# Optimization experiments

Measured on AMD Instinct MI355X. Metric: run time of the kernel, lower is better.

## Reference

```python
import jax, jax.numpy as jnp
import numpy as np

N, E, B = 524288, 4194304, 16384
F_IN, FP, TV, GOUT = 14, 1024, 256, 32
EPS = 1e-5
SLOPE = 0.2  # PyG GATConv default negative_slope


def setup_inputs() -> dict:
    key = jax.random.key(0)
    ks = iter(jax.random.split(key, 64))
    def nrm(shape, scale=1.0):
        return jax.random.normal(next(ks), shape, dtype=jnp.float32) * scale
    def uni(shape, lo, hi):
        return jax.random.uniform(next(ks), shape, dtype=jnp.float32, minval=lo, maxval=hi)
    def bn(d):  # [gamma, beta, running_mean, running_var]
        return jnp.stack([uni((d,), 0.5, 1.5), nrm((d,), 0.1), nrm((d,), 0.1), uni((d,), 0.5, 1.5)])
    return {
        'x': nrm((N, F_IN)),
        'edge_index': jax.random.randint(next(ks), (2, E), 0, N, dtype=jnp.int32),
        'batch': jnp.sort(jax.random.randint(next(ks), (N,), 0, B, dtype=jnp.int32)),
        'fingerprint': nrm((B, FP)),
        'transformer_features': nrm((B, TV)),
        'W1': nrm((F_IN, F_IN), 0.3), 'a_src1': nrm((F_IN,), 0.3), 'a_dst1': nrm((F_IN,), 0.3), 'b1': nrm((F_IN,), 0.1),
        'W2': nrm((F_IN, GOUT), 0.3), 'a_src2': nrm((GOUT,), 0.3), 'a_dst2': nrm((GOUT,), 0.3), 'b2': nrm((GOUT,), 0.1),
        'fc1_w': nrm((FP, 400), 0.04), 'fc1_b': nrm((400,), 0.1), 'bn1': bn(400),
        'fc2_w': nrm((400, 200), 0.07), 'fc2_b': nrm((200,), 0.1), 'bn2': bn(200),
        'fc3_w': nrm((TV, 400), 0.08), 'fc3_b': nrm((400,), 0.1), 'bn3': bn(400),
        'fc4_w': nrm((400, 200), 0.07), 'fc4_b': nrm((200,), 0.1), 'bn4': bn(200),
        'fcc1_w': nrm((GOUT + 400, 100), 0.07), 'fcc1_b': nrm((100,), 0.1), 'bnc': bn(100),
        'fcc2_w': nrm((100, 1), 0.1), 'fcc2_b': nrm((1,), 0.1),
    }


def _bn(h, p):  # eval-mode BatchNorm1d with packed params [4, d]
    return (h - p[2]) * jax.lax.rsqrt(p[3] + EPS) * p[0] + p[1]


def _gat(x, W, a_s, a_d, b, src, dst, n):
    # PyG GATConv, heads=1: messages flow src -> dst, softmax over incoming edges per dst
    h = x @ W                                   # [n, C]
    e = jax.nn.leaky_relu((h @ a_s)[src] + (h @ a_d)[dst], SLOPE)  # [E_tot]
    m = jax.lax.stop_gradient(jax.ops.segment_max(e, dst, num_segments=n))
    w = jnp.exp(e - m[dst])
    denom = jax.ops.segment_sum(w, dst, num_segments=n)
    alpha = w / denom[dst]
    out = jax.ops.segment_sum(alpha[:, None] * h[src], dst, num_segments=n)
    return out + b


def reference(x, edge_index, batch, fingerprint, transformer_features,
              W1, a_src1, a_dst1, b1, W2, a_src2, a_dst2, b2,
              fc1_w, fc1_b, bn1, fc2_w, fc2_b, bn2,
              fc3_w, fc3_b, bn3, fc4_w, fc4_b, bn4,
              fcc1_w, fcc1_b, bnc, fcc2_w, fcc2_b):
    n = x.shape[0]
    loop = jnp.arange(n, dtype=edge_index.dtype)  # add_self_loops
    src = jnp.concatenate([edge_index[0], loop])
    dst = jnp.concatenate([edge_index[1], loop])
    g = jax.nn.relu(_gat(x, W1, a_src1, a_dst1, b1, src, dst, n))
    g = jax.nn.relu(_gat(g, W2, a_src2, a_dst2, b2, src, dst, n))
    pool = jax.ops.segment_sum(g, batch, num_segments=B)  # global_add_pool -> [B, GOUT]
    fp = jax.nn.relu(_bn(fingerprint @ fc1_w + fc1_b, bn1))
    fp = jax.nn.relu(_bn(fp @ fc2_w + fc2_b, bn2))
    tv = jax.nn.relu(_bn(transformer_features @ fc3_w + fc3_b, bn3))
    tv = jax.nn.relu(_bn(tv @ fc4_w + fc4_b, bn4))
    comb = jnp.concatenate([pool, fp, tv], axis=1)  # [B, 32+200+200]
    comb = jax.nn.relu(_bn(comb @ fcc1_w + fcc1_b, bnc))
    return comb @ fcc2_w + fcc2_b  # [B, 1]
```

## Files before the change

### kernel.cpp

```cpp
#include <hip/hip_runtime.h>

typedef unsigned short u16;
typedef unsigned int u32;
typedef __attribute__((ext_vector_type(8))) short bf16x8;
typedef __attribute__((ext_vector_type(4))) float f32x4;

#define N_NODES 524288
#define N_EDGES 4194304
#define N_GRAPH 16384
#define P_BLOCKS 1024
#define BKTS 512
#define DPB 1024
#define CAP 8960
#define TTOT 2825
#define LBLK 2048

__device__ __forceinline__ float bf2f(u16 u){ u32 x=((u32)u)<<16; float f; __builtin_memcpy(&f,&x,4); return f; }
__device__ __forceinline__ float lo2f(u32 u){ u32 x=u<<16; float f; __builtin_memcpy(&f,&x,4); return f; }
__device__ __forceinline__ float hi2f(u32 u){ u32 x=u&0xffff0000u; float f; __builtin_memcpy(&f,&x,4); return f; }
__device__ __forceinline__ u16 f2bf(float f){ u32 x; __builtin_memcpy(&x,&f,4); return (u16)((x + 0x7fffu + ((x>>16)&1u))>>16); }
__device__ __forceinline__ float lrelu(float e){ return e>0.f? e : 0.2f*e; }
__device__ __forceinline__ float gload(const void* p, int i, int is32){
    return is32 ? ((const float*)p)[i] : bf2f(((const u16*)p)[i]);
}
__device__ __forceinline__ u32 fmax_key(float f){ u32 u; __builtin_memcpy(&u,&f,4); return (u>>31)? ~u : (u|0x80000000u); }
__device__ __forceinline__ float key_fmax(u32 k){ u32 u = (k>>31)? (k^0x80000000u) : ~k; float f; __builtin_memcpy(&f,&u,4); return f; }

__device__ __forceinline__ void edge_acc(uint4 q0, uint4 q1, float adv, float M,
        float* acc, float& den){
    float as_; __builtin_memcpy(&as_, &q1.w, 4);
    float w = __expf(lrelu(as_ + adv) - M); den += w;
    u32 u[7] = {q0.x,q0.y,q0.z,q0.w,q1.x,q1.y,q1.z};
    #pragma unroll
    for (int f=0;f<14;f++){ u32 uu=u[f>>1]; acc[f] += w*((f&1)? hi2f(uu):lo2f(uu)); }
}

__device__ __forceinline__ void walk8(const int* __restrict__ ssrc, const u16* __restrict__ hsrc,
        int beg, int end, float adv, float M, float* acc, float& den){
    for (int j = beg; j < end; j += 8){
        int s8[8];
        #pragma unroll
        for (int k=0;k<8;k++){
            int e = j + k;
            s8[k] = __builtin_nontemporal_load(ssrc + ((e < end) ? e : (end-1)));
        }
        uint4 r0[8], r1[8];
        #pragma unroll
        for (int k=0;k<8;k++){
            const uint4* hp = (const uint4*)(hsrc + (size_t)s8[k]*16);
            r0[k] = hp[0]; r1[k] = hp[1];
        }
        int m = end - j;
        #pragma unroll
        for (int k=0;k<8;k++) if (k < m) edge_acc(r0[k], r1[k], adv, M, acc, den);
    }
}

__device__ __forceinline__ void gemm_block(u16 (*As)[40], u16 (*Bs)[40],
        const void* __restrict__ A, const u16* __restrict__ Wt,
        const void* __restrict__ bias, const void* __restrict__ bnp, void* __restrict__ out,
        int K, int Kp, int Nc, int ostride, int ooff, int do_relu,
        int out32, int araw, int is32, int bm, int bn, int t){
    int af32 = araw && is32;
    int lane = t & 63, wave = t >> 6;
    int mt = (wave & 1) * 64, nt = (wave >> 1) * 64;
    int quad = lane >> 4, fr = lane & 15;

    f32x4 zero = {0.f, 0.f, 0.f, 0.f};
    f32x4 acc[4][4];
    #pragma unroll
    for (int i=0;i<4;i++)
        #pragma unroll
        for (int j=0;j<4;j++) acc[i][j] = zero;

    int srow0 = t >> 2;
    int scol = (t & 3) * 8;

    for (int k0 = 0; k0 < Kp; k0 += 32){
        #pragma unroll
        for (int h2_=0; h2_<2; h2_++){
            int row = srow0 + h2_*64;
            int gk = k0 + scol;
            uint4 av = make_uint4(0,0,0,0);
            if (gk + 8 <= K){
                if (af32){
                    const float* ap = (const float*)A + (size_t)(bm+row)*K + gk;
                    float4 a0 = *(const float4*)ap, a1 = *(const float4*)(ap+4);
                    av.x = (u32)f2bf(a0.x) | ((u32)f2bf(a0.y)<<16);
                    av.y = (u32)f2bf(a0.z) | ((u32)f2bf(a0.w)<<16);
                    av.z = (u32)f2bf(a1.x) | ((u32)f2bf(a1.y)<<16);
                    av.w = (u32)f2bf(a1.z) | ((u32)f2bf(a1.w)<<16);
                } else {
                    av = *(const uint4*)((const u16*)A + (size_t)(bm+row)*K + gk);
                }
            }
            *(uint4*)(&As[row][scol]) = av;
            uint4 bv = make_uint4(0,0,0,0);
            if (bn + row < Nc) bv = *(const uint4*)(Wt + (size_t)(bn+row)*Kp + gk);
            *(uint4*)(&Bs[row][scol]) = bv;
        }
        __syncthreads();
        bf16x8 af[4], bfr[4];
        #pragma unroll
        for (int i=0;i<4;i++) af[i] = *(const bf16x8*)(&As[mt + i*16 + fr][quad*8]);
        #pragma unroll
        for (int j=0;j<4;j++) bfr[j] = *(const bf16x8*)(&Bs[nt + j*16 + fr][quad*8]);
        #pragma unroll
        for (int i=0;i<4;i++)
            #pragma unroll
            for (int j=0;j<4;j++)
                acc[i][j] = __builtin_amdgcn_mfma_f32_16x16x32_bf16(af[i], bfr[j], acc[i][j], 0, 0, 0);
        __syncthreads();
    }

    #pragma unroll
    for (int j=0;j<4;j++){
        int gn = bn + nt + j*16 + fr;
        if (gn >= Nc) continue;
        float bb = gload(bias, gn, is32);
        float scale = 1.f, shift = bb;
        if (bnp){
            float gm_ = gload(bnp, gn, is32), bt = gload(bnp, Nc+gn, is32);
            float mn = gload(bnp, 2*Nc+gn, is32), vr = gload(bnp, 3*Nc+gn, is32);
            scale = gm_ * rsqrtf(vr + 1e-5f);
            shift = (bb - mn)*scale + bt;
        }
        #pragma unroll
        for (int i=0;i<4;i++){
            #pragma unroll
            for (int r=0;r<4;r++){
                int gm = bm + mt + i*16 + quad*4 + r;
                float v = acc[i][j][r]*scale + shift;
                if (do_relu) v = fmaxf(v, 0.f);
                size_t oidx = (size_t)gm*ostride + ooff + gn;
                if (out32) ((float*)out)[oidx] = v;
                else       ((u16*)out)[oidx] = f2bf(v);
            }
        }
    }
}

__global__ __launch_bounds__(256) void k_detect(const u32* __restrict__ x, int* __restrict__ flag,
        const void* __restrict__ W2, const void* __restrict__ asw, const void* __restrict__ adw,
        float* __restrict__ prep){
    __shared__ int cnt, s32;
    int t = threadIdx.x;
    if (t==0) cnt = 0;
    __syncthreads();
    int c = 0;
    for (int i = t; i < 1024; i += 256){
        u32 e = (x[i] >> 7) & 0xFF;
        if (e >= 110 && e <= 140) c++;
    }
    atomicAdd(&cnt, c);
    __syncthreads();
    if (t==0){ int f = (cnt < 512) ? 1 : 0; *flag = f; s32 = f; }
    __syncthreads();
    int is32 = s32;
    if (t < 28){
        int j = t % 14, which = t / 14;
        const void* av = which ? adw : asw;
        float s = 0.f;
        #pragma unroll
        for (int k=0;k<32;k++) s += gload(W2, j*32+k, is32) * gload(av, k, is32);
        prep[which*14 + j] = s;
    }
}

__global__ __launch_bounds__(256) void k_p1t(const int* __restrict__ dst, u32* __restrict__ tbl_bm,
        const void* __restrict__ Wa, const void* __restrict__ Wb, const void* __restrict__ Wc,
        const void* __restrict__ Wd, const void* __restrict__ We,
        u16* __restrict__ Ta, u16* __restrict__ Tb, u16* __restrict__ Tc,
        u16* __restrict__ Td, u16* __restrict__ Te, const int* __restrict__ flag,
        const void* __restrict__ x, const void* __restrict__ W1,
        const void* __restrict__ asw, const void* __restrict__ adw,
        u16* __restrict__ h1, float* __restrict__ ad1, u32* __restrict__ gkey){
    __shared__ u32 lh[BKTS];
    __shared__ float Wf[196], av14[14], dv14[14];
    __shared__ float red[256];
    int bid = blockIdx.x, t = threadIdx.x;
    if (bid >= P_BLOCKS + TTOT){
        int is32 = *flag;
        if (t < 196) Wf[t] = gload(W1, t, is32);
        else if (t < 210) av14[t-196] = gload(asw, t-196, is32);
        else if (t < 224) dv14[t-210] = gload(adw, t-210, is32);
        __syncthreads();
        int i = (bid - P_BLOCKS - TTOT)*256 + t;
        float xv[14];
        if (is32){
            const float* xr = (const float*)x + (size_t)i*14;
            #pragma unroll
            for (int k=0;k<14;k++) xv[k] = xr[k];
        } else {
            const u32* xr = (const u32*)((const u16*)x + (size_t)i*14);
            #pragma unroll
            for (int p=0;p<7;p++){ u32 u = xr[p]; xv[2*p]=lo2f(u); xv[2*p+1]=hi2f(u); }
        }
        float h[14];
        #pragma unroll
        for (int j=0;j<14;j++){ float s=0.f;
            #pragma unroll
            for (int k=0;k<14;k++) s += xv[k]*Wf[k*14+j];
            h[j]=s; }
        float a=0.f, d=0.f;
        #pragma unroll
        for (int j=0;j<14;j++){ a += h[j]*av14[j]; d += h[j]*dv14[j]; }
        ad1[i]=d;
        u32 ou[8];
        #pragma unroll
        for (int p=0;p<7;p++) ou[p] = (u32)f2bf(h[2*p]) | ((u32)f2bf(h[2*p+1])<<16);
        __builtin_memcpy(&ou[7], &a, 4);
        uint4* hp = (uint4*)(h1 + (size_t)i*16);
        hp[0] = make_uint4(ou[0],ou[1],ou[2],ou[3]);
        hp[1] = make_uint4(ou[4],ou[5],ou[6],ou[7]);
        red[t] = a; __syncthreads();
        for (int o=128;o;o>>=1){ if (t<o) red[t]=fmaxf(red[t],red[t+o]); __syncthreads(); }
        if (t==0) atomicMax(gkey, fmax_key(red[0]));
        return;
    }
    if (bid >= P_BLOCKS){
        int is32 = *flag;
        int loc = (bid - P_BLOCKS)*256 + t;
        const int n1=400*1024, n2=200*416, n3=400*256, n4=200*416, n5=100*448;
        const void* W; u16* T; int K, Kp, Nc;
        if (loc < n1){ W=Wa; T=Ta; K=1024; Kp=1024; Nc=400; }
        else if ((loc-=n1) < n2){ W=Wb; T=Tb; K=400; Kp=416; Nc=200; }
        else if ((loc-=n2) < n3){ W=Wc; T=Tc; K=256; Kp=256; Nc=400; }
        else if ((loc-=n3) < n4){ W=Wd; T=Td; K=400; Kp=416; Nc=200; }
        else if ((loc-=n4) < n5){ W=We; T=Te; K=432; Kp=448; Nc=100; }
        else return;
        int n = loc / Kp, k = loc - n*Kp;
        T[loc] = (k < K) ? f2bf(gload(W, k*Nc + n, is32)) : (u16)0;
        return;
    }
    int blk = bid;
    lh[t] = 0; lh[t+256] = 0;
    __syncthreads();
    int base = blk*4096;
    #pragma unroll
    for (int k=0;k<16;k++){
        int d = __builtin_nontemporal_load(dst + base + k*256 + t) & (N_NODES-1);
        atomicAdd(&lh[d>>10], 1);
    }
    __syncthreads();
    tbl_bm[blk*BKTS + t]       = lh[t];
    tbl_bm[blk*BKTS + t + 256] = lh[t+256];
}

__global__ __launch_bounds__(256) void k_ttbl(const u32* __restrict__ bm, u32* __restrict__ km){
    __shared__ u32 tile[32][33];
    int bx = blockIdx.x, by = blockIdx.y;
    int tx = threadIdx.x & 31, ty = threadIdx.x >> 5;
    #pragma unroll
    for (int r=0;r<32;r+=8)
        tile[ty+r][tx] = bm[(bx*32 + ty + r)*BKTS + by*32 + tx];
    __syncthreads();
    #pragma unroll
    for (int r=0;r<32;r+=8)
        km[(by*32 + ty + r)*P_BLOCKS + bx*32 + tx] = tile[tx][ty+r];
}

__global__ __launch_bounds__(256) void k_scan1(int* __restrict__ data, int* __restrict__ bsums){
    __shared__ int sh[256];
    int b = blockIdx.x, t = threadIdx.x;
    int base = b*1024 + t*4;
    int4 v = *(const int4*)(data + base);
    int s = v.x+v.y+v.z+v.w;
    sh[t] = s; __syncthreads();
    for (int off=1; off<256; off<<=1){
        int xv = (t>=off)? sh[t-off] : 0; __syncthreads();
        sh[t] += xv; __syncthreads();
    }
    int excl = sh[t] - s;
    if (t==255) bsums[b] = sh[255];
    int4 o; o.x = excl; o.y = excl+v.x; o.z = o.y+v.y; o.w = o.z+v.z;
    *(int4*)(data + base) = o;
}

__global__ __launch_bounds__(256) void k_scan2(int* __restrict__ bsums){
    __shared__ int sh[256];
    int t = threadIdx.x;
    int v0 = bsums[2*t], v1 = bsums[2*t+1];
    int s = v0+v1; sh[t] = s; __syncthreads();
    for (int off=1; off<256; off<<=1){
        int xv = (t>=off)? sh[t-off] : 0; __syncthreads();
        sh[t] += xv; __syncthreads();
    }
    int excl = sh[t] - s;
    bsums[2*t] = excl; bsums[2*t+1] = excl + v0;
}

__global__ __launch_bounds__(256) void k_scan3(int* __restrict__ scan, const int* __restrict__ bsums, int N_, int E_){
    int i = blockIdx.x*256 + threadIdx.x;
    if (i < N_) scan[i] += bsums[i>>10];
    if (i == 0) scan[N_] = E_;
}

__global__ __launch_bounds__(256) void k_p2(const int* __restrict__ src, const int* __restrict__ dst,
        const u32* __restrict__ km, u32* __restrict__ btab){
    __shared__ u32 lh[BKTS], lofs[BKTS], gofs[BKTS];
    __shared__ u32 stage[4096], tgt[4096];
    __shared__ u32 red[256];
    int t = threadIdx.x, blk = blockIdx.x;
    lh[t] = 0; lh[t+256] = 0;
    __syncthreads();
    u32 pr[16], rk[16]; u16 bk[16];
    int base = blk*4096;
    #pragma unroll
    for (int k=0;k<16;k++){
        int e = base + k*256 + t;
        int d = __builtin_nontemporal_load(dst+e) & (N_NODES-1);
        int s = __builtin_nontemporal_load(src+e) & (N_NODES-1);
        u32 b = (u32)d >> 10;
        bk[k] = (u16)b;
        pr[k] = (u32)(d & 1023) | ((u32)s << 10);
        rk[k] = atomicAdd(&lh[b], 1);
    }
    gofs[t]       = km[(size_t)t*P_BLOCKS + blk];
    gofs[t+256]   = km[(size_t)(t+256)*P_BLOCKS + blk];
    __syncthreads();
    u32 v0 = lh[2*t], v1 = lh[2*t+1];
    u32 s2 = v0+v1; red[t] = s2; __syncthreads();
    for (int off=1; off<256; off<<=1){
        u32 xv = (t>=off)? red[t-off] : 0; __syncthreads();
        red[t] += xv; __syncthreads();
    }
    u32 excl = red[t] - s2;
    lofs[2*t] = excl; lofs[2*t+1] = excl + v0;
    __syncthreads();
    #pragma unroll
    for (int k=0;k<16;k++){
        u32 p = lofs[bk[k]] + rk[k];
        stage[p] = pr[k];
        tgt[p]   = gofs[bk[k]] + rk[k];
    }
    __syncthreads();
    #pragma unroll
    for (int k=0;k<16;k++){
        int j = k*256 + t;
        btab[tgt[j]] = stage[j];
    }
}

__global__ __launch_bounds__(256) void k_p3(const u32* __restrict__ km, const u32* __restrict__ btab,
        int* __restrict__ rowptr, int* __restrict__ ssrc){
    __shared__ u32 fh[DPB], fo[DPB];
    __shared__ u32 red[256];
    __shared__ int sst[CAP];
    int t = threadIdx.x, b = blockIdx.x;
    u32 basep = km[(size_t)b*P_BLOCKS];
    u32 endp  = km[(size_t)(b+1)*P_BLOCKS];
    int cnt = (int)(endp - basep);
    #pragma unroll
    for (int i=t;i<DPB;i+=256) fh[i] = 0;
    __syncthreads();
    for (int j=t; j<cnt; j+=256){
        u32 p = btab[basep + j];
        atomicAdd(&fh[p & 1023], 1);
    }
    __syncthreads();
    u32 v0=fh[4*t], v1=fh[4*t+1], v2=fh[4*t+2], v3=fh[4*t+3];
    u32 s4 = v0+v1+v2+v3; red[t] = s4; __syncthreads();
    for (int off=1; off<256; off<<=1){
        u32 xv = (t>=off)? red[t-off] : 0; __syncthreads();
        red[t] += xv; __syncthreads();
    }
    u32 excl = red[t] - s4;
    fo[4*t]=excl; fo[4*t+1]=excl+v0; fo[4*t+2]=excl+v0+v1; fo[4*t+3]=excl+v0+v1+v2;
    __syncthreads();
    #pragma unroll
    for (int i=t;i<DPB;i+=256) rowptr[b*DPB + i] = (int)(basep + fo[i]);
    if (b == BKTS-1 && t == 0) rowptr[N_NODES] = (int)endp;
    __syncthreads();
    for (int j=t; j<cnt; j+=256){
        u32 p = btab[basep + j];
        u32 pos = atomicAdd(&fo[p & 1023], 1);
        if (pos < (u32)CAP) sst[pos] = (int)(p >> 10);
    }
    __syncthreads();
    for (int j=t; j<cnt; j+=256) ssrc[basep + j] = sst[j];
}

__global__ __launch_bounds__(256) void k_g1mlp(const int* __restrict__ rowptr, const int* __restrict__ ssrc,
        const u16* __restrict__ h1, const float* __restrict__ ad1, const u32* __restrict__ gkey1,
        const void* __restrict__ b1, const float* __restrict__ prep,
        u16* __restrict__ g1, float* __restrict__ ad2, u32* __restrict__ gkey2,
        const int* __restrict__ flag,
        const void* __restrict__ fing, const u16* __restrict__ Wt1,
        const void* __restrict__ fc1b, const void* __restrict__ bn1, u16* __restrict__ fp1,
        const void* __restrict__ tv, const u16* __restrict__ Wt3,
        const void* __restrict__ fc3b, const void* __restrict__ bn3, u16* __restrict__ tv1){
    __shared__ u16 As[128][40];
    __shared__ u16 Bs[128][40];
    __shared__ float b1s[14], vas[14], vds[14];
    __shared__ float red[256];
    int is32 = *flag;
    int bid = blockIdx.x, t = threadIdx.x;
    if (bid % 3 == 0){
        int g = bid / 3;
        int gg = (g < 512) ? g : g - 512;
        int r = gg & 7, q = gg >> 3;
        int bn = (q & 3) * 128;
        int bm = ((q >> 2) * 8 + r) * 128;
        if (g < 512)
            gemm_block(As, Bs, fing, Wt1, fc1b, bn1, fp1, 1024, 1024, 400, 400, 0, 1, 0,
                       1, is32, bm, bn, t);
        else
            gemm_block(As, Bs, tv, Wt3, fc3b, bn3, tv1, 256, 256, 400, 400, 0, 1, 0,
                       1, is32, bm, bn, t);
        return;
    }
    int gb = bid - bid/3 - 1;
    if (t < 14) b1s[t] = gload(b1, t, is32);
    else if (t < 28) vas[t-14] = prep[t-14];
    else if (t < 42) vds[t-28] = prep[t-28+14];
    __syncthreads();
    int i = gb*256 + t;
    float adv = ad1[i];
    float M = lrelu(key_fmax(*gkey1) + adv);
    int beg = rowptr[i], end = rowptr[i+1];
    float acc[14] = {0,0,0,0,0,0,0,0,0,0,0,0,0,0};
    float den = 0.f;
    {
        const uint4* hp = (const uint4*)(h1 + (size_t)i*16);
        edge_acc(hp[0], hp[1], adv, M, acc, den);
    }
    walk8(ssrc, h1, beg, end, adv, M, acc, den);
    float inv = 1.0f/den;
    float v[14];
    #pragma unroll
    for (int f=0;f<14;f++) v[f] = fmaxf(acc[f]*inv + b1s[f], 0.f);
    float a2=0.f, d2=0.f;
    #pragma unroll
    for (int f=0;f<14;f++){ a2 += v[f]*vas[f]; d2 += v[f]*vds[f]; }
    ad2[i] = d2;
    u32 ou[8];
    #pragma unroll
    for (int p=0;p<7;p++) ou[p] = (u32)f2bf(v[2*p]) | ((u32)f2bf(v[2*p+1])<<16);
    __builtin_memcpy(&ou[7], &a2, 4);
    uint4* gp = (uint4*)(g1 + (size_t)i*16);
    gp[0]=make_uint4(ou[0],ou[1],ou[2],ou[3]);
    gp[1]=make_uint4(ou[4],ou[5],ou[6],ou[7]);
    red[t] = a2; __syncthreads();
    for (int o=128;o;o>>=1){ if (t<o) red[t]=fmaxf(red[t],red[t+o]); __syncthreads(); }
    if (t==0) atomicMax(gkey2, fmax_key(red[0]));
}

__global__ __launch_bounds__(256) void k_g2mlp(const int* __restrict__ rowptr, const int* __restrict__ ssrc,
        const u16* __restrict__ g1, const float* __restrict__ ad2, const u32* __restrict__ gkey2,
        const void* __restrict__ W2, const void* __restrict__ b2, u16* __restrict__ g2,
        const int* __restrict__ flag,
        const u16* __restrict__ fp1, const u16* __restrict__ Wt2,
        const void* __restrict__ fc2b, const void* __restrict__ bn2,
        const u16* __restrict__ tv1, const u16* __restrict__ Wt4,
        const void* __restrict__ fc4b, const void* __restrict__ bn4,
        u16* __restrict__ comb){
    __shared__ u16 As[128][40];
    __shared__ u16 Bs[128][40];
    __shared__ float W2s[448], b2s[32];
    int is32 = *flag;
    int bid = blockIdx.x, t = threadIdx.x;
    if (bid % 5 == 0){
        int g = bid / 5;
        int gg = (g < 256) ? g : g - 256;
        int r = gg & 7, q = gg >> 3;
        int bn = (q & 1) * 128;
        int bm = ((q >> 1) * 8 + r) * 128;
        if (g < 256)
            gemm_block(As, Bs, fp1, Wt2, fc2b, bn2, comb, 400, 416, 200, 432, 32, 1, 0,
                       0, is32, bm, bn, t);
        else
            gemm_block(As, Bs, tv1, Wt4, fc4b, bn4, comb, 400, 416, 200, 432, 232, 1, 0,
                       0, is32, bm, bn, t);
        return;
    }
    int gb = bid - bid/5 - 1;
    for (int idx=t; idx<448; idx+=256) W2s[idx] = gload(W2, idx, is32);
    if (t < 32) b2s[t] = gload(b2, t, is32);
    __syncthreads();
    int i = gb*256 + t;
    float adv = ad2[i];
    float M = lrelu(key_fmax(*gkey2) + adv);
    int beg = rowptr[i], end = rowptr[i+1];
    float acc[14] = {0,0,0,0,0,0,0,0,0,0,0,0,0,0};
    float den = 0.f;
    {
        const uint4* hp = (const uint4*)(g1 + (size_t)i*16);
        edge_acc(hp[0], hp[1], adv, M, acc, den);
    }
    walk8(ssrc, g1, beg, end, adv, M, acc, den);
    float inv = 1.0f/den;
    float an[14];
    #pragma unroll
    for (int f=0;f<14;f++) an[f] = acc[f]*inv;
    uint4* orow = (uint4*)(g2 + (size_t)i*32);
    #pragma unroll
    for (int g=0; g<4; g++){
        u32 ou[4];
        #pragma unroll
        for (int p=0;p<4;p++){
            int j0 = g*8 + 2*p;
            float va_ = b2s[j0], vb_ = b2s[j0+1];
            #pragma unroll
            for (int k=0;k<14;k++){ va_ += an[k]*W2s[k*32+j0]; vb_ += an[k]*W2s[k*32+j0+1]; }
            va_ = fmaxf(va_, 0.f); vb_ = fmaxf(vb_, 0.f);
            ou[p] = (u32)f2bf(va_) | ((u32)f2bf(vb_)<<16);
        }
        orow[g] = make_uint4(ou[0],ou[1],ou[2],ou[3]);
    }
}

__device__ __forceinline__ int lbound(const int* __restrict__ a, int n, int v){
    int lo=0, hi=n;
    while (lo < hi){ int m = (lo+hi)>>1; if (a[m] < v) lo = m+1; else hi = m; }
    return lo;
}

__global__ __launch_bounds__(64) void k_pool(const u16* __restrict__ g2, const int* __restrict__ batch,
        u16* __restrict__ comb, int N_){
    int b = blockIdx.x;
    int t = threadIdx.x, f = t & 31, half = t >> 5;
    int lo = lbound(batch, N_, b);
    int hi = lbound(batch, N_, b+1);
    float acc = 0.f;
    for (int i = lo + half; i < hi; i += 2) acc += bf2f(g2[(size_t)i*32 + f]);
    acc += __shfl_xor(acc, 32);
    if (t < 32) comb[(size_t)b*432 + f] = f2bf(acc);
}

__global__ __launch_bounds__(256) void k_gemm(const void* __restrict__ A, const u16* __restrict__ Wt,
        const void* __restrict__ bias, const void* __restrict__ bnp, void* __restrict__ out,
        int K, int Kp, int Nc, int ostride, int ooff, int do_relu,
        int out32, int araw, const int* __restrict__ flag){
    __shared__ u16 As[128][40];
    __shared__ u16 Bs[128][40];
    int is32 = *flag;
    gemm_block(As, Bs, A, Wt, bias, bnp, out, K, Kp, Nc, ostride, ooff, do_relu, out32,
               araw, is32, blockIdx.x*128, blockIdx.y*128, threadIdx.x);
}

__global__ __launch_bounds__(256) void k_fcc2(const float* __restrict__ c1, const void* __restrict__ w,
        const void* __restrict__ b, float* __restrict__ outp, const int* __restrict__ flag){
    int is32 = *flag;
    __shared__ float wf[100];
    int t = threadIdx.x;
    if (t < 100) wf[t] = gload(w, t, is32);
    __syncthreads();
    int i = blockIdx.x*256 + t;
    const float* r = c1 + (size_t)i*100;
    float s = 0.f;
    #pragma unroll 4
    for (int k=0;k<100;k++) s += r[k]*wf[k];
    outp[i] = s + gload(b, 0, is32);
}

extern "C" void kernel_launch(void* const* d_in, const int* in_sizes, int n_in,
                              void* d_out, int out_size, void* d_ws, size_t ws_size,
                              hipStream_t stream){
    const int N = N_NODES, E = N_EDGES;
    const void* x    = d_in[0];
    const int* ei   = (const int*)d_in[1];
    const int* srcA = ei;
    const int* dstA = ei + E;
    const int* batch= (const int*)d_in[2];
    const void* fing = d_in[3];
    const void* tv   = d_in[4];
    const void* W1   = d_in[5];
    const void* as1w = d_in[6];
    const void* ad1w = d_in[7];
    const void* b1   = d_in[8];
    const void* W2   = d_in[9];
    const void* as2w = d_in[10];
    const void* ad2w = d_in[11];
    const void* b2   = d_in[12];
    const void* fc1w = d_in[13]; const void* fc1b = d_in[14]; const void* bn1 = d_in[15];
    const void* fc2w = d_in[16]; const void* fc2b = d_in[17]; const void* bn2 = d_in[18];
    const void* fc3w = d_in[19]; const void* fc3b = d_in[20]; const void* bn3 = d_in[21];
    const void* fc4w = d_in[22]; const void* fc4b = d_in[23]; const void* bn4 = d_in[24];
    const void* fccw = d_in[25]; const void* fccb = d_in[26]; const void* bnc = d_in[27];
    const void* fcc2w= d_in[28]; const void* fcc2b= d_in[29];

    char* ws = (char*)d_ws;
    size_t off = 0;
    auto alloc = [&](size_t bytes)->char*{ char* p = ws + off; off = (off + bytes + 255) & ~(size_t)255; return p; };
    int*  flagp  = (int*)alloc(256);
    u32*  gkey1  = (u32*)flagp + 1;
    u32*  gkey2  = (u32*)flagp + 2;
    float* prep  = (float*)((char*)flagp + 16);
    int*  rowptr = (int*)alloc((size_t)(N+1)*4);
    int*  bsums  = (int*)alloc(513*4);
    u32*  tbl_bm = (u32*)alloc((size_t)BKTS*P_BLOCKS*4);
    u32*  tbl_km = (u32*)alloc(((size_t)BKTS*P_BLOCKS+1)*4);
    int*  ssrc   = (int*)alloc((size_t)E*4);
    u16*  h1     = (u16*)alloc((size_t)N*16*2);
    u16*  g1     = (u16*)alloc((size_t)N*16*2);
    float* ad1_  = (float*)alloc((size_t)N*4);
    float* ad2_  = (float*)alloc((size_t)N*4);
    char* scr32  = alloc((size_t)N*32*2);
    float* c1    = (float*)alloc((size_t)N_GRAPH*100*4);
    u16*  Wt1    = (u16*)alloc((size_t)400*1024*2);
    u16*  Wt2    = (u16*)alloc((size_t)200*416*2);
    u16*  Wt3    = (u16*)alloc((size_t)400*256*2);
    u16*  Wt4    = (u16*)alloc((size_t)200*416*2);
    u16*  Wtc    = (u16*)alloc((size_t)100*448*2);
    u16*  fp1    = (u16*)alloc((size_t)N_GRAPH*400*2);
    u16*  tv1    = (u16*)alloc((size_t)N_GRAPH*400*2);
    u32*  btab   = (u32*)scr32;
    u16*  g2     = (u16*)scr32;
    u16*  comb   = (u16*)h1;

    (void)hipMemsetAsync(flagp, 0, 256, stream);

    k_detect <<<1, 256, 0, stream>>>((const u32*)x, flagp, W2, as2w, ad2w, prep);

    k_p1t  <<<P_BLOCKS + TTOT + LBLK, 256, 0, stream>>>(dstA, tbl_bm,
                 fc1w, fc2w, fc3w, fc4w, fccw, Wt1, Wt2, Wt3, Wt4, Wtc, flagp,
                 x, W1, as1w, ad1w, h1, ad1_, gkey1);
    k_ttbl <<<dim3(32,16), 256, 0, stream>>>(tbl_bm, tbl_km);
    k_scan1<<<512,  256, 0, stream>>>((int*)tbl_km, bsums);
    k_scan2<<<1,    256, 0, stream>>>(bsums);
    k_scan3<<<(BKTS*P_BLOCKS)/256, 256, 0, stream>>>((int*)tbl_km, bsums, BKTS*P_BLOCKS, E);
    k_p2   <<<P_BLOCKS, 256, 0, stream>>>(srcA, dstA, tbl_km, btab);
    k_p3   <<<BKTS, 256, 0, stream>>>(tbl_km, btab, rowptr, ssrc);

    k_g1mlp <<<3072, 256, 0, stream>>>(rowptr, ssrc, h1, ad1_, gkey1, b1, prep, g1, ad2_, gkey2, flagp,
                                       fing, Wt1, fc1b, bn1, fp1,
                                       tv,   Wt3, fc3b, bn3, tv1);
    k_g2mlp <<<2560, 256, 0, stream>>>(rowptr, ssrc, g1, ad2_, gkey2, W2, b2, g2, flagp,
                                       fp1, Wt2, fc2b, bn2,
                                       tv1, Wt4, fc4b, bn4, comb);
    k_pool   <<<N_GRAPH, 64, 0, stream>>>(g2, batch, comb, N);

    k_gemm<<<dim3(128,1), 256, 0, stream>>>(comb, Wtc, fccb, bnc, c1,  432, 448, 100, 100,   0, 1, 1, 0, flagp);

    k_fcc2<<<N_GRAPH/256, 256, 0, stream>>>(c1, fcc2w, fcc2b, (float*)d_out, flagp);
}
```

Baseline: 630.4 us.

## Fuse scan fixup with table transpose and fuse final GEMM with fcc2 head

Replaces the scan-offset fixup kernel with a tiled transpose that adds the block sums and writes a bucket-major-by-block table. This lets k_p2 read its 512 offsets contiguously instead of strided, and k_p3 read bucket starts directly. It also fuses the fcc1 GEMM+BN+ReLU with the final 100->1 dot product via LDS atomics, which removes the c1 intermediate and one launch. The cost is an extra table buffer and shared-memory atomic contention in the epilogue.

```diff
diff --git a/kernel.cpp b/kernel.cpp
--- a/kernel.cpp
+++ b/kernel.cpp
@@ -290,14 +290,24 @@
     bsums[2*t] = excl; bsums[2*t+1] = excl + v0;
 }
 
-__global__ __launch_bounds__(256) void k_scan3(int* __restrict__ scan, const int* __restrict__ bsums, int N_, int E_){
-    int i = blockIdx.x*256 + threadIdx.x;
-    if (i < N_) scan[i] += bsums[i>>10];
-    if (i == 0) scan[N_] = E_;
+__global__ __launch_bounds__(256) void k_tfix(const u32* __restrict__ km, const int* __restrict__ bsums,
+        u32* __restrict__ kmT){
+    __shared__ u32 tile[32][33];
+    int bx = blockIdx.x, by = blockIdx.y;
+    int tx = threadIdx.x & 31, ty = threadIdx.x >> 5;
+    #pragma unroll
+    for (int r=0;r<32;r+=8){
+        int bucket = by*32 + ty + r;
+        tile[ty+r][tx] = km[(size_t)bucket*P_BLOCKS + bx*32 + tx] + (u32)bsums[bucket];
+    }
+    __syncthreads();
+    #pragma unroll
+    for (int r=0;r<32;r+=8)
+        kmT[(size_t)(bx*32 + ty + r)*BKTS + by*32 + tx] = tile[tx][ty+r];
 }
 
 __global__ __launch_bounds__(256) void k_p2(const int* __restrict__ src, const int* __restrict__ dst,
-        const u32* __restrict__ km, u32* __restrict__ btab){
+        const u32* __restrict__ kmT, u32* __restrict__ btab){
     __shared__ u32 lh[BKTS], lofs[BKTS], gofs[BKTS];
     __shared__ u32 stage[4096], tgt[4096];
     __shared__ u32 red[256];
@@ -316,8 +326,8 @@
         pr[k] = (u32)(d & 1023) | ((u32)s << 10);
         rk[k] = atomicAdd(&lh[b], 1);
     }
-    gofs[t]       = km[(size_t)t*P_BLOCKS + blk];
-    gofs[t+256]   = km[(size_t)(t+256)*P_BLOCKS + blk];
+    gofs[t]       = kmT[(size_t)blk*BKTS + t];
+    gofs[t+256]   = kmT[(size_t)blk*BKTS + t + 256];
     __syncthreads();
     u32 v0 = lh[2*t], v1 = lh[2*t+1];
     u32 s2 = v0+v1; red[t] = s2; __syncthreads();
@@ -342,14 +352,14 @@
     }
 }
 
-__global__ __launch_bounds__(256) void k_p3(const u32* __restrict__ km, const u32* __restrict__ btab,
+__global__ __launch_bounds__(256) void k_p3(const u32* __restrict__ kmT, const u32* __restrict__ btab,
         int* __restrict__ rowptr, int* __restrict__ ssrc){
     __shared__ u32 fh[DPB], fo[DPB];
     __shared__ u32 red[256];
     __shared__ int sst[CAP];
     int t = threadIdx.x, b = blockIdx.x;
-    u32 basep = km[(size_t)b*P_BLOCKS];
-    u32 endp  = km[(size_t)(b+1)*P_BLOCKS];
+    u32 basep = kmT[b];
+    u32 endp  = (b == BKTS-1) ? (u32)N_EDGES : kmT[b+1];
     int cnt = (int)(endp - basep);
     #pragma unroll
     for (int i=t;i<DPB;i+=256) fh[i] = 0;
@@ -528,30 +538,82 @@
     if (t < 32) comb[(size_t)b*432 + f] = f2bf(acc);
 }
 
-__global__ __launch_bounds__(256) void k_gemm(const void* __restrict__ A, const u16* __restrict__ Wt,
-        const void* __restrict__ bias, const void* __restrict__ bnp, void* __restrict__ out,
-        int K, int Kp, int Nc, int ostride, int ooff, int do_relu,
-        int out32, int araw, const int* __restrict__ flag){
+__global__ __launch_bounds__(256) void k_gemmfin(const u16* __restrict__ A, const u16* __restrict__ Wt,
+        const void* __restrict__ bias, const void* __restrict__ bnp,
+        const void* __restrict__ w2, const void* __restrict__ b2,
+        float* __restrict__ outp, const int* __restrict__ flag){
     __shared__ u16 As[128][40];
     __shared__ u16 Bs[128][40];
+    __shared__ float wf[100];
+    __shared__ float rowacc[128];
     int is32 = *flag;
-    gemm_block(As, Bs, A, Wt, bias, bnp, out, K, Kp, Nc, ostride, ooff, do_relu, out32,
-               araw, is32, blockIdx.x*128, blockIdx.y*128, threadIdx.x);
-}
-
-__global__ __launch_bounds__(256) void k_fcc2(const float* __restrict__ c1, const void* __restrict__ w,
-        const void* __restrict__ b, float* __restrict__ outp, const int* __restrict__ flag){
-    int is32 = *flag;
-    __shared__ float wf[100];
     int t = threadIdx.x;
-    if (t < 100) wf[t] = gload(w, t, is32);
-    __syncthreads();
-    int i = blockIdx.x*256 + t;
-    const float* r = c1 + (size_t)i*100;
-    float s = 0.f;
-    #pragma unroll 4
-    for (int k=0;k<100;k++) s += r[k]*wf[k];
-    outp[i] = s + gload(b, 0, is32);
+    const int K = 432, Kp = 448, Nc = 100;
+    if (t < 100) wf[t] = gload(w2, t, is32);
+    if (t < 128) rowacc[t] = 0.f;
+    int lane = t & 63, wave = t >> 6;
+    int bm = blockIdx.x * 128;
+    int mt = (wave & 1) * 64, nt = (wave >> 1) * 64;
+    int quad = lane >> 4, fr = lane & 15;
+
+    f32x4 zero = {0.f, 0.f, 0.f, 0.f};
+    f32x4 acc[4][4];
+    #pragma unroll
+    for (int i=0;i<4;i++)
+        #pragma unroll
+        for (int j=0;j<4;j++) acc[i][j] = zero;
+
+    int srow0 = t >> 2;
+    int scol = (t & 3) * 8;
+
+    for (int k0 = 0; k0 < Kp; k0 += 32){
+        #pragma unroll
+        for (int h2_=0; h2_<2; h2_++){
+            int row = srow0 + h2_*64;
+            int gk = k0 + scol;
+            uint4 av = make_uint4(0,0,0,0);
+            if (gk + 8 <= K) av = *(const uint4*)(A + (size_t)(bm+row)*K + gk);
+            *(uint4*)(&As[row][scol]) = av;
+            uint4 bv = make_uint4(0,0,0,0);
+            if (row < Nc) bv = *(const uint4*)(Wt + (size_t)row*Kp + gk);
+            *(uint4*)(&Bs[row][scol]) = bv;
+        }
+        __syncthreads();
+        bf16x8 af[4], bfr[4];
+        #pragma unroll
+        for (int i=0;i<4;i++) af[i] = *(const bf16x8*)(&As[mt + i*16 + fr][quad*8]);
+        #pragma unroll
+        for (int j=0;j<4;j++) bfr[j] = *(const bf16x8*)(&Bs[nt + j*16 + fr][quad*8]);
+        #pragma unroll
+        for (int i=0;i<4;i++)
+            #pragma unroll
+            for (int j=0;j<4;j++)
+                acc[i][j] = __builtin_amdgcn_mfma_f32_16x16x32_bf16(af[i], bfr[j], acc[i][j], 0, 0, 0);
+        __syncthreads();
+    }
+
+    #pragma unroll
+    for (int j=0;j<4;j++){
+        int gn = nt + j*16 + fr;
+        if (gn >= Nc) continue;
+        float bb = gload(bias, gn, is32);
+        float gm_ = gload(bnp, gn, is32), bt = gload(bnp, Nc+gn, is32);
+        float mn = gload(bnp, 2*Nc+gn, is32), vr = gload(bnp, 3*Nc+gn, is32);
+        float scale = gm_ * rsqrtf(vr + 1e-5f);
+        float shift = (bb - mn)*scale + bt;
+        float wgn = wf[gn];
+        #pragma unroll
+        for (int i=0;i<4;i++){
+            #pragma unroll
+            for (int r=0;r<4;r++){
+                int lgm = mt + i*16 + quad*4 + r;
+                float v = fmaxf(acc[i][j][r]*scale + shift, 0.f);
+                atomicAdd(&rowacc[lgm], v*wgn);
+            }
+        }
+    }
+    __syncthreads();
+    if (t < 128) outp[bm + t] = rowacc[t] + gload(b2, 0, is32);
 }
 
 extern "C" void kernel_launch(void* const* d_in, const int* in_sizes, int n_in,
@@ -591,13 +653,13 @@
     int*  bsums  = (int*)alloc(513*4);
     u32*  tbl_bm = (u32*)alloc((size_t)BKTS*P_BLOCKS*4);
     u32*  tbl_km = (u32*)alloc(((size_t)BKTS*P_BLOCKS+1)*4);
+    u32*  kmT    = (u32*)alloc((size_t)BKTS*P_BLOCKS*4);
     int*  ssrc   = (int*)alloc((size_t)E*4);
     u16*  h1     = (u16*)alloc((size_t)N*16*2);
     u16*  g1     = (u16*)alloc((size_t)N*16*2);
     float* ad1_  = (float*)alloc((size_t)N*4);
     float* ad2_  = (float*)alloc((size_t)N*4);
     char* scr32  = alloc((size_t)N*32*2);
-    float* c1    = (float*)alloc((size_t)N_GRAPH*100*4);
     u16*  Wt1    = (u16*)alloc((size_t)400*1024*2);
     u16*  Wt2    = (u16*)alloc((size_t)200*416*2);
     u16*  Wt3    = (u16*)alloc((size_t)400*256*2);
@@ -619,9 +681,9 @@
     k_ttbl <<<dim3(32,16), 256, 0, stream>>>(tbl_bm, tbl_km);
     k_scan1<<<512,  256, 0, stream>>>((int*)tbl_km, bsums);
     k_scan2<<<1,    256, 0, stream>>>(bsums);
-    k_scan3<<<(BKTS*P_BLOCKS)/256, 256, 0, stream>>>((int*)tbl_km, bsums, BKTS*P_BLOCKS, E);
-    k_p2   <<<P_BLOCKS, 256, 0, stream>>>(srcA, dstA, tbl_km, btab);
-    k_p3   <<<BKTS, 256, 0, stream>>>(tbl_km, btab, rowptr, ssrc);
+    k_tfix <<<dim3(32,16), 256, 0, stream>>>(tbl_km, bsums, kmT);
+    k_p2   <<<P_BLOCKS, 256, 0, stream>>>(srcA, dstA, kmT, btab);
+    k_p3   <<<BKTS, 256, 0, stream>>>(kmT, btab, rowptr, ssrc);
 
     k_g1mlp <<<3072, 256, 0, stream>>>(rowptr, ssrc, h1, ad1_, gkey1, b1, prep, g1, ad2_, gkey2, flagp,
                                        fing, Wt1, fc1b, bn1, fp1,
@@ -631,7 +693,5 @@
                                        tv1, Wt4, fc4b, bn4, comb);
     k_pool   <<<N_GRAPH, 64, 0, stream>>>(g2, batch, comb, N);
 
-    k_gemm<<<dim3(128,1), 256, 0, stream>>>(comb, Wtc, fccb, bnc, c1,  432, 448, 100, 100,   0, 1, 1, 0, flagp);
-
-    k_fcc2<<<N_GRAPH/256, 256, 0, stream>>>(c1, fcc2w, fcc2b, (float*)d_out, flagp);
-}
+    k_gemmfin<<<128, 256, 0, stream>>>(comb, Wtc, fccb, bnc, fcc2w, fcc2b, (float*)d_out, flagp);
+}
```

Measured after the change: 646.3 us. 1.03x slower.
